# Kernel tuning notes

Hardware: AMD Instinct MI355X
Metric: run time of the kernel (lower is better)

The kernel has to match this reference:

```python
import jax, jax.numpy as jnp
import numpy as np

N = 8192
E = 262144
D_IN = 128
D_OUT = 128

def setup_inputs() -> dict:
    key = jax.random.key(0)
    k1, k2, k3, k4 = jax.random.split(key, 4)
    x = jax.random.normal(k1, (N, D_IN), dtype=jnp.float32)
    edge_index = jax.random.randint(k2, (2, E), 0, N, dtype=jnp.int64)
    W = jax.random.normal(k3, (D_OUT, D_IN), dtype=jnp.float32) * 0.05
    b = jax.random.normal(k4, (D_OUT,), dtype=jnp.float32) * 0.05
    return {"x": x, "edge_index": edge_index, "W": W, "b": b}

def reference(x, edge_index, W, b):
    num_nodes = x.shape[0]
    # Dense adjacency: adj[src, dst] = 1.0 (duplicate edges set, not add)
    adj = jnp.zeros((num_nodes, num_nodes), dtype=x.dtype)
    adj = adj.at[edge_index[0], edge_index[1]].set(1.0)
    adj = adj + jnp.eye(num_nodes, dtype=x.dtype)  # self-loops (added on top)
    degree = adj.sum(axis=1, keepdims=True)
    degree = jnp.where(degree > 0, degree, jnp.ones_like(degree))
    adj = adj / degree  # row-normalize
    out = adj @ x               # [N, D_IN] aggregation
    out = out @ W.T + b         # nn.Linear
    return out
```

## Files before the change

### kernel.cpp

```cpp
#include <hip/hip_runtime.h>


typedef unsigned int uint32;

#define NNODES 8192
#define DF 128
#define WPR 256
#define M 4
#define CAP 192

__global__ void edge_scatter(const int* __restrict__ ei, int E,
                             uint32* __restrict__ bm) {
    int e = blockIdx.x * blockDim.x + threadIdx.x;
    if (e >= E) return;
    int src = ei[e];
    int dst = ei[E + e];
    atomicOr(&bm[(size_t)src * WPR + (dst >> 5)], 1u << (dst & 31));
}

__global__ __launch_bounds__(128) void gcn_fused(
    const float* __restrict__ x,
    const uint32* __restrict__ bm,
    const float4* __restrict__ zrow,
    const float* __restrict__ W,
    const float* __restrict__ b,
    float* __restrict__ out)
{
    __shared__ int nbr[M][CAP];
    __shared__ int cnt_s[M];
    __shared__ __align__(16) float part[M][4][DF];
    __shared__ float agg[M][DF];

    const int t    = threadIdx.x;
    const int lane = t & 63;
    const int wv   = t >> 6;
    const int node0 = blockIdx.x * M;

    #pragma unroll
    for (int pass = 0; pass < 2; ++pass) {
        const int m = pass * 2 + wv;
        const uint32* r = bm + (size_t)(node0 + m) * WPR;
        uint32 w0 = r[4 * lane + 0], w1 = r[4 * lane + 1],
               w2 = r[4 * lane + 2], w3 = r[4 * lane + 3];
        int c = __popc(w0) + __popc(w1) + __popc(w2) + __popc(w3);
        int v = c;
        #pragma unroll
        for (int d = 1; d < 64; d <<= 1) {
            int up = __shfl_up(v, d);
            if (lane >= d) v += up;
        }
        int off = v - c;
        if (lane == 63) cnt_s[m] = v;
        uint32 ws[4] = {w0, w1, w2, w3};
        #pragma unroll
        for (int q = 0; q < 4; ++q) {
            uint32 word = ws[q];
            int base = (4 * lane + q) << 5;
            while (word) {
                int bit = __ffs(word) - 1; word &= word - 1;
                if (off < CAP) nbr[m][off] = base + bit;
                off++;
            }
        }
    }
    __syncthreads();

    const int c0 = cnt_s[0], c1 = cnt_s[1], c2 = cnt_s[2], c3 = cnt_s[3];
    int Lmax = max(max(c0, c1), max(c2, c3));
    const bool overflow = (Lmax > CAP);
    int L = (min(Lmax, CAP) + 3) & ~3;

    for (int m = 0; m < M; ++m) {
        int cm = min(cnt_s[m], CAP);
        for (int k = cm + t; k < L; k += 128) nbr[m][k] = -1;
    }
    __syncthreads();

    if (!overflow) {
        const int g = t >> 5;
        const int c = t & 31;
        const float4* x4 = (const float4*)x;

        float4 acc[M];
        #pragma unroll
        for (int m = 0; m < M; ++m) acc[m] = make_float4(0.f, 0.f, 0.f, 0.f);

        for (int k = g; k < L; k += 4) {
            #pragma unroll
            for (int m = 0; m < M; ++m) {
                int j = nbr[m][k];
                const float4* p = (j >= 0) ? (x4 + (size_t)j * (DF / 4) + c)
                                           : (zrow + c);
                float4 vx = *p;
                acc[m].x += vx.x; acc[m].y += vx.y;
                acc[m].z += vx.z; acc[m].w += vx.w;
            }
        }

        #pragma unroll
        for (int m = 0; m < M; ++m)
            *(float4*)&part[m][g][c * 4] = acc[m];
        __syncthreads();

        #pragma unroll
        for (int m = 0; m < M; ++m) {
            float s = part[m][0][t] + part[m][1][t]
                    + part[m][2][t] + part[m][3][t];
            s += x[(size_t)(node0 + m) * DF + t];
            agg[m][t] = s / (float)(1 + cnt_s[m]);
        }
    } else {
        for (int m = 0; m < M; ++m) {
            const uint32* r = bm + (size_t)(node0 + m) * WPR;
            float acc = x[(size_t)(node0 + m) * DF + t];
            for (int w = 0; w < WPR; ++w) {
                uint32 word = r[w];
                int base = w << 5;
                while (word) {
                    int bit = __ffs(word) - 1; word &= word - 1;
                    acc += x[(size_t)(base + bit) * DF + t];
                }
            }
            agg[m][t] = acc / (float)(1 + cnt_s[m]);
        }
    }
    __syncthreads();

    const float4* Wrow = (const float4*)(W + (size_t)t * DF);
    float bias = b[t];
    float sum[M];
    #pragma unroll
    for (int m = 0; m < M; ++m) sum[m] = bias;

    #pragma unroll 8
    for (int c4 = 0; c4 < DF / 4; ++c4) {
        float4 wvv = Wrow[c4];
        #pragma unroll
        for (int m = 0; m < M; ++m) {
            sum[m] += wvv.x * agg[m][c4 * 4 + 0] + wvv.y * agg[m][c4 * 4 + 1]
                    + wvv.z * agg[m][c4 * 4 + 2] + wvv.w * agg[m][c4 * 4 + 3];
        }
    }
    #pragma unroll
    for (int m = 0; m < M; ++m)
        out[(size_t)(node0 + m) * DF + t] = sum[m];
}

extern "C" void kernel_launch(void* const* d_in, const int* in_sizes, int n_in,
                              void* d_out, int out_size, void* d_ws, size_t ws_size,
                              hipStream_t stream) {
    const float* x = (const float*)d_in[0];
    const int*  ei = (const int*)d_in[1];
    const float* W = (const float*)d_in[2];
    const float* b = (const float*)d_in[3];
    float* out = (float*)d_out;

    uint32* bm = (uint32*)d_ws;
    const size_t bm_bytes = (size_t)NNODES * WPR * sizeof(uint32);
    const float4* zrow = (const float4*)((char*)d_ws + bm_bytes);
    const int E = in_sizes[1] / 2;

    hipMemsetAsync(d_ws, 0, bm_bytes + DF * sizeof(float), stream);

    edge_scatter<<<dim3((E + 255) / 256), dim3(256), 0, stream>>>(ei, E, bm);
    gcn_fused<<<dim3(NNODES / M), dim3(128), 0, stream>>>(x, bm, zrow, W, b, out);
}
```

Baseline: 100.4 us.

## Process eight nodes per 256-thread block, vectorize edge scatter and bitmap loads

The fused kernel now handles eight nodes per block with 256 threads, with each half-block aggregating and projecting four nodes. Each half loops only to its own nodes' padded neighbour counts instead of the block-wide maximum, and padding is limited to the next multiple of four. The edge scatter loads four edges per thread with int4 reads, and bitmap rows are read as uint4. This aims to cut wasted gather iterations and per-edge load overhead, at the cost of an int4 alignment assumption and a serial tail loop for leftover edges.

Result: slower. 106.8 us (+6.4%).

```diff
diff --git a/kernel.cpp b/kernel.cpp
--- a/kernel.cpp
+++ b/kernel.cpp
@@ -6,19 +6,31 @@
 #define NNODES 8192
 #define DF 128
 #define WPR 256
-#define M 4
+#define M 8
 #define CAP 192
 
 __global__ void edge_scatter(const int* __restrict__ ei, int E,
                              uint32* __restrict__ bm) {
-    int e = blockIdx.x * blockDim.x + threadIdx.x;
-    if (e >= E) return;
-    int src = ei[e];
-    int dst = ei[E + e];
-    atomicOr(&bm[(size_t)src * WPR + (dst >> 5)], 1u << (dst & 31));
+    int e4 = blockIdx.x * blockDim.x + threadIdx.x;
+    int E4 = E >> 2;
+    if (e4 < E4) {
+        const int4* s4 = (const int4*)ei;
+        const int4* d4 = (const int4*)(ei + E);
+        int4 s = s4[e4], d = d4[e4];
+        atomicOr(&bm[(size_t)s.x * WPR + (d.x >> 5)], 1u << (d.x & 31));
+        atomicOr(&bm[(size_t)s.y * WPR + (d.y >> 5)], 1u << (d.y & 31));
+        atomicOr(&bm[(size_t)s.z * WPR + (d.z >> 5)], 1u << (d.z & 31));
+        atomicOr(&bm[(size_t)s.w * WPR + (d.w >> 5)], 1u << (d.w & 31));
+    }
+    if (e4 == 0) {
+        for (int e = E & ~3; e < E; ++e) {
+            int src = ei[e], dst = ei[E + e];
+            atomicOr(&bm[(size_t)src * WPR + (dst >> 5)], 1u << (dst & 31));
+        }
+    }
 }
 
-__global__ __launch_bounds__(128) void gcn_fused(
+__global__ __launch_bounds__(256) void gcn_fused(
     const float* __restrict__ x,
     const uint32* __restrict__ bm,
     const float4* __restrict__ zrow,
@@ -38,20 +50,19 @@
 
     #pragma unroll
     for (int pass = 0; pass < 2; ++pass) {
-        const int m = pass * 2 + wv;
-        const uint32* r = bm + (size_t)(node0 + m) * WPR;
-        uint32 w0 = r[4 * lane + 0], w1 = r[4 * lane + 1],
-               w2 = r[4 * lane + 2], w3 = r[4 * lane + 3];
-        int c = __popc(w0) + __popc(w1) + __popc(w2) + __popc(w3);
+        const int m = pass * 4 + wv;
+        const uint4* r = (const uint4*)(bm + (size_t)(node0 + m) * WPR);
+        uint4 w = r[lane];
+        int c = __popc(w.x) + __popc(w.y) + __popc(w.z) + __popc(w.w);
         int v = c;
         #pragma unroll
-        for (int d = 1; d < 64; d <<= 1) {
-            int up = __shfl_up(v, d);
-            if (lane >= d) v += up;
+        for (int dd = 1; dd < 64; dd <<= 1) {
+            int up = __shfl_up(v, dd);
+            if (lane >= dd) v += up;
         }
         int off = v - c;
         if (lane == 63) cnt_s[m] = v;
-        uint32 ws[4] = {w0, w1, w2, w3};
+        uint32 ws[4] = {w.x, w.y, w.z, w.w};
         #pragma unroll
         for (int q = 0; q < 4; ++q) {
             uint32 word = ws[q];
@@ -65,85 +76,104 @@
     }
     __syncthreads();
 
-    const int c0 = cnt_s[0], c1 = cnt_s[1], c2 = cnt_s[2], c3 = cnt_s[3];
-    int Lmax = max(max(c0, c1), max(c2, c3));
-    const bool overflow = (Lmax > CAP);
-    int L = (min(Lmax, CAP) + 3) & ~3;
+    int cnt[M];
+    int allmax = 0;
+    #pragma unroll
+    for (int m = 0; m < M; ++m) { cnt[m] = cnt_s[m]; allmax = max(allmax, cnt[m]); }
+    const bool overflow = (allmax > CAP);
 
-    for (int m = 0; m < M; ++m) {
-        int cm = min(cnt_s[m], CAP);
-        for (int k = cm + t; k < L; k += 128) nbr[m][k] = -1;
+    if (t < M) {
+        int cm = min(cnt_s[t], CAP);
+        int c4 = (cm + 3) & ~3;
+        for (int k = cm; k < c4; ++k) nbr[t][k] = -1;
     }
     __syncthreads();
 
+    const int half = t >> 7;
+    const int d    = t & 127;
+
     if (!overflow) {
-        const int g = t >> 5;
+        const int g = (t >> 5) & 3;
         const int c = t & 31;
         const float4* x4 = (const float4*)x;
 
-        float4 acc[M];
+        int c4v[4];
+        int Lwp = 0;
         #pragma unroll
-        for (int m = 0; m < M; ++m) acc[m] = make_float4(0.f, 0.f, 0.f, 0.f);
+        for (int i = 0; i < 4; ++i) {
+            int cm = min(cnt[4 * half + i], CAP);
+            c4v[i] = (cm + 3) & ~3;
+            Lwp = max(Lwp, c4v[i]);
+        }
 
-        for (int k = g; k < L; k += 4) {
+        float4 acc[4];
+        #pragma unroll
+        for (int i = 0; i < 4; ++i) acc[i] = make_float4(0.f, 0.f, 0.f, 0.f);
+
+        for (int k = g; k < Lwp; k += 4) {
             #pragma unroll
-            for (int m = 0; m < M; ++m) {
-                int j = nbr[m][k];
-                const float4* p = (j >= 0) ? (x4 + (size_t)j * (DF / 4) + c)
-                                           : (zrow + c);
-                float4 vx = *p;
-                acc[m].x += vx.x; acc[m].y += vx.y;
-                acc[m].z += vx.z; acc[m].w += vx.w;
+            for (int i = 0; i < 4; ++i) {
+                if (k < c4v[i]) {
+                    int j = nbr[4 * half + i][k];
+                    const float4* p = (j >= 0) ? (x4 + (size_t)j * (DF / 4) + c)
+                                               : (zrow + c);
+                    float4 vx = *p;
+                    acc[i].x += vx.x; acc[i].y += vx.y;
+                    acc[i].z += vx.z; acc[i].w += vx.w;
+                }
             }
         }
 
         #pragma unroll
-        for (int m = 0; m < M; ++m)
-            *(float4*)&part[m][g][c * 4] = acc[m];
+        for (int i = 0; i < 4; ++i)
+            *(float4*)&part[4 * half + i][g][c * 4] = acc[i];
         __syncthreads();
 
         #pragma unroll
-        for (int m = 0; m < M; ++m) {
-            float s = part[m][0][t] + part[m][1][t]
-                    + part[m][2][t] + part[m][3][t];
-            s += x[(size_t)(node0 + m) * DF + t];
-            agg[m][t] = s / (float)(1 + cnt_s[m]);
+        for (int i = 0; i < 4; ++i) {
+            int m = 4 * half + i;
+            float s = part[m][0][d] + part[m][1][d]
+                    + part[m][2][d] + part[m][3][d];
+            s += x[(size_t)(node0 + m) * DF + d];
+            agg[m][d] = s / (float)(1 + cnt[m]);
         }
     } else {
-        for (int m = 0; m < M; ++m) {
+        for (int i = 0; i < 4; ++i) {
+            int m = 4 * half + i;
             const uint32* r = bm + (size_t)(node0 + m) * WPR;
-            float acc = x[(size_t)(node0 + m) * DF + t];
+            float acc = x[(size_t)(node0 + m) * DF + d];
             for (int w = 0; w < WPR; ++w) {
                 uint32 word = r[w];
                 int base = w << 5;
                 while (word) {
                     int bit = __ffs(word) - 1; word &= word - 1;
-                    acc += x[(size_t)(base + bit) * DF + t];
+                    acc += x[(size_t)(base + bit) * DF + d];
                 }
             }
-            agg[m][t] = acc / (float)(1 + cnt_s[m]);
+            agg[m][d] = acc / (float)(1 + cnt[m]);
         }
     }
     __syncthreads();
 
-    const float4* Wrow = (const float4*)(W + (size_t)t * DF);
-    float bias = b[t];
-    float sum[M];
+    const float4* Wrow = (const float4*)(W + (size_t)d * DF);
+    float bias = b[d];
+    float sum[4];
     #pragma unroll
-    for (int m = 0; m < M; ++m) sum[m] = bias;
+    for (int i = 0; i < 4; ++i) sum[i] = bias;
 
     #pragma unroll 8
-    for (int c4 = 0; c4 < DF / 4; ++c4) {
-        float4 wvv = Wrow[c4];
+    for (int c4i = 0; c4i < DF / 4; ++c4i) {
+        float4 wvv = Wrow[c4i];
         #pragma unroll
-        for (int m = 0; m < M; ++m) {
-            sum[m] += wvv.x * agg[m][c4 * 4 + 0] + wvv.y * agg[m][c4 * 4 + 1]
-                    + wvv.z * agg[m][c4 * 4 + 2] + wvv.w * agg[m][c4 * 4 + 3];
+        for (int i = 0; i < 4; ++i) {
+            const float* a = &agg[4 * half + i][c4i * 4];
+            sum[i] += wvv.x * a[0] + wvv.y * a[1]
+                    + wvv.z * a[2] + wvv.w * a[3];
         }
     }
     #pragma unroll
-    for (int m = 0; m < M; ++m)
-        out[(size_t)(node0 + m) * DF + t] = sum[m];
+    for (int i = 0; i < 4; ++i)
+        out[(size_t)(node0 + 4 * half + i) * DF + d] = sum[i];
 }
 
 extern "C" void kernel_launch(void* const* d_in, const int* in_sizes, int n_in,
@@ -162,6 +192,7 @@
 
     hipMemsetAsync(d_ws, 0, bm_bytes + DF * sizeof(float), stream);
 
-    edge_scatter<<<dim3((E + 255) / 256), dim3(256), 0, stream>>>(ei, E, bm);
-    gcn_fused<<<dim3(NNODES / M), dim3(128), 0, stream>>>(x, bm, zrow, W, b, out);
+    int E4 = E >> 2;
+    edge_scatter<<<dim3((E4 + 255) / 256), dim3(256), 0, stream>>>(ei, E, bm);
+    gcn_fused<<<dim3(NNODES / M), dim3(256), 0, stream>>>(x, bm, zrow, W, b, out);
 }
```

## Replace global adjacency bitmap with per-node edge buckets and shared-memory dedup

Applied to the files above, without the earlier changes.

Drops the 8 MB global bitmap and its memset. Edges now go into fixed-capacity per-source buckets through atomicAdd counters, and the fused kernel removes duplicates with a shared-memory bitmap before building neighbour lists. The aim is to cut memset and bitmap read traffic, but it adds shared-memory atomics and unordered neighbour lists, plus an edge-list scan fallback for any node with more than CAP edges. The scatter kernel also touches x to warm it into cache before the fused kernel runs.

Result: slower. 103.0 us (+2.5%).

```diff
diff --git a/kernel.cpp b/kernel.cpp
--- a/kernel.cpp
+++ b/kernel.cpp
@@ -5,74 +5,87 @@
 
 #define NNODES 8192
 #define DF 128
-#define WPR 256
 #define M 4
 #define CAP 192
+#define NTHR 128
+#define WPN 256
 
-__global__ void edge_scatter(const int* __restrict__ ei, int E,
-                             uint32* __restrict__ bm) {
+__global__ void bucket_scatter(const int* __restrict__ ei, int E,
+                               int* __restrict__ cntg, int* __restrict__ bkt,
+                               const float4* __restrict__ x4) {
     int e = blockIdx.x * blockDim.x + threadIdx.x;
-    if (e >= E) return;
-    int src = ei[e];
-    int dst = ei[E + e];
-    atomicOr(&bm[(size_t)src * WPR + (dst >> 5)], 1u << (dst & 31));
+    if (e < E) {
+        int src = ei[e];
+        int dst = ei[E + e];
+        int pos = atomicAdd(&cntg[src], 1);
+        if (pos < CAP) bkt[(size_t)src * CAP + pos] = dst;
+    }
+    if (e < NNODES * DF / 4) {
+        float4 px = x4[e];
+        asm volatile("" :: "v"(px.x), "v"(px.y), "v"(px.z), "v"(px.w));
+    }
 }
 
 __global__ __launch_bounds__(128) void gcn_fused(
     const float* __restrict__ x,
-    const uint32* __restrict__ bm,
+    const int* __restrict__ ei, int E,
+    const int* __restrict__ cntg,
+    const int* __restrict__ bkt,
     const float4* __restrict__ zrow,
     const float* __restrict__ W,
     const float* __restrict__ b,
     float* __restrict__ out)
 {
     __shared__ int nbr[M][CAP];
+    __shared__ uint32 lbm[M][WPN];
     __shared__ int cnt_s[M];
+    __shared__ int ovf_s[M];
     __shared__ __align__(16) float part[M][4][DF];
     __shared__ float agg[M][DF];
 
-    const int t    = threadIdx.x;
-    const int lane = t & 63;
-    const int wv   = t >> 6;
+    const int t     = threadIdx.x;
     const int node0 = blockIdx.x * M;
 
+    for (int i = t; i < M * WPN; i += NTHR) ((uint32*)lbm)[i] = 0;
+    if (t < M) { cnt_s[t] = 0; ovf_s[t] = 0; }
+    __syncthreads();
+
     #pragma unroll
-    for (int pass = 0; pass < 2; ++pass) {
-        const int m = pass * 2 + wv;
-        const uint32* r = bm + (size_t)(node0 + m) * WPR;
-        uint32 w0 = r[4 * lane + 0], w1 = r[4 * lane + 1],
-               w2 = r[4 * lane + 2], w3 = r[4 * lane + 3];
-        int c = __popc(w0) + __popc(w1) + __popc(w2) + __popc(w3);
-        int v = c;
-        #pragma unroll
-        for (int d = 1; d < 64; d <<= 1) {
-            int up = __shfl_up(v, d);
-            if (lane >= d) v += up;
-        }
-        int off = v - c;
-        if (lane == 63) cnt_s[m] = v;
-        uint32 ws[4] = {w0, w1, w2, w3};
-        #pragma unroll
-        for (int q = 0; q < 4; ++q) {
-            uint32 word = ws[q];
-            int base = (4 * lane + q) << 5;
-            while (word) {
-                int bit = __ffs(word) - 1; word &= word - 1;
-                if (off < CAP) nbr[m][off] = base + bit;
-                off++;
+    for (int m = 0; m < M; ++m) {
+        const int node = node0 + m;
+        const int raw = cntg[node];
+        if (raw <= CAP) {
+            for (int k = t; k < raw; k += NTHR) {
+                int dst = bkt[(size_t)node * CAP + k];
+                uint32 bit = 1u << (dst & 31);
+                uint32 old = atomicOr(&lbm[m][dst >> 5], bit);
+                if (!(old & bit)) {
+                    int pos = atomicAdd(&cnt_s[m], 1);
+                    nbr[m][pos] = dst;
+                }
+            }
+        } else {
+            if (t == 0) ovf_s[m] = 1;
+            for (int e = t; e < E; e += NTHR) {
+                if (ei[e] == node) {
+                    int dst = ei[E + e];
+                    uint32 bit = 1u << (dst & 31);
+                    uint32 old = atomicOr(&lbm[m][dst >> 5], bit);
+                    if (!(old & bit)) atomicAdd(&cnt_s[m], 1);
+                }
             }
         }
     }
     __syncthreads();
 
+    const bool overflow = (ovf_s[0] | ovf_s[1] | ovf_s[2] | ovf_s[3]) != 0;
     const int c0 = cnt_s[0], c1 = cnt_s[1], c2 = cnt_s[2], c3 = cnt_s[3];
     int Lmax = max(max(c0, c1), max(c2, c3));
-    const bool overflow = (Lmax > CAP);
     int L = (min(Lmax, CAP) + 3) & ~3;
 
     for (int m = 0; m < M; ++m) {
         int cm = min(cnt_s[m], CAP);
-        for (int k = cm + t; k < L; k += 128) nbr[m][k] = -1;
+        for (int k = cm + t; k < L; k += NTHR) nbr[m][k] = -1;
     }
     __syncthreads();
 
@@ -111,10 +124,9 @@
         }
     } else {
         for (int m = 0; m < M; ++m) {
-            const uint32* r = bm + (size_t)(node0 + m) * WPR;
             float acc = x[(size_t)(node0 + m) * DF + t];
-            for (int w = 0; w < WPR; ++w) {
-                uint32 word = r[w];
+            for (int w = 0; w < WPN; ++w) {
+                uint32 word = lbm[m][w];
                 int base = w << 5;
                 while (word) {
                     int bit = __ffs(word) - 1; word &= word - 1;
@@ -155,13 +167,16 @@
     const float* b = (const float*)d_in[3];
     float* out = (float*)d_out;
 
-    uint32* bm = (uint32*)d_ws;
-    const size_t bm_bytes = (size_t)NNODES * WPR * sizeof(uint32);
-    const float4* zrow = (const float4*)((char*)d_ws + bm_bytes);
+    int* cntg = (int*)d_ws;
+    const size_t cnt_bytes  = (size_t)NNODES * sizeof(int);
+    const float4* zrow = (const float4*)((char*)d_ws + cnt_bytes);
+    int* bkt = (int*)((char*)d_ws + cnt_bytes + 512);
     const int E = in_sizes[1] / 2;
 
-    hipMemsetAsync(d_ws, 0, bm_bytes + DF * sizeof(float), stream);
+    hipMemsetAsync(d_ws, 0, cnt_bytes + 512, stream);
 
-    edge_scatter<<<dim3((E + 255) / 256), dim3(256), 0, stream>>>(ei, E, bm);
-    gcn_fused<<<dim3(NNODES / M), dim3(128), 0, stream>>>(x, bm, zrow, W, b, out);
+    bucket_scatter<<<dim3((E + 255) / 256), dim3(256), 0, stream>>>(
+        ei, E, cntg, bkt, (const float4*)x);
+    gcn_fused<<<dim3(NNODES / M), dim3(NTHR), 0, stream>>>(
+        x, ei, E, cntg, bkt, zrow, W, b, out);
 }
```
